# Optimization experiments

Measured on AMD Instinct MI355X. Metric: run time of the kernel, lower is better.

Reference implementation:

```python
import jax, jax.numpy as jnp
import numpy as np

B, N, NPOINT, NSAMPLE, C = 8, 8192, 2048, 32, 64
RADIUS = 0.2
MLP = [C + 3, 64, 64, 128]  # use_xyz=True -> C+3 input channels


def setup_inputs() -> dict:
    key = jax.random.key(0)
    ks = jax.random.split(key, 8)
    xyz = jax.random.normal(ks[0], (B, N, 3), jnp.float32)
    features = jax.random.normal(ks[1], (B, C, N), jnp.float32)
    inp = {"xyz": xyz, "features": features}
    # shared-MLP (1x1 conv) weights, He-init
    for i in range(3):
        cin, cout = MLP[i], MLP[i + 1]
        scale = jnp.sqrt(jnp.float32(2.0) / cin)
        inp[f"W{i+1}"] = jax.random.normal(ks[2 + i], (cout, cin), jnp.float32) * scale
        inp[f"b{i+1}"] = jnp.zeros((cout,), jnp.float32)
    return inp


def furthest_point_sample(xyz, npoint):
    # xyz: (B, N, 3) -> idx: (B, npoint). Greedy FPS, seeded at point 0 (as CUDA impl).
    b, n, _ = xyz.shape

    def step(carry, _):
        dist, far = carry  # dist: (B, N) running min dist-to-set; far: (B,)
        centroid = jnp.take_along_axis(xyz, far[:, None, None], axis=1)  # (B,1,3)
        d = jnp.sum((xyz - centroid) ** 2, axis=-1)  # (B, N)
        dist = jnp.minimum(dist, d)
        nxt = jnp.argmax(dist, axis=-1).astype(jnp.int32)
        return (dist, nxt), far

    init = (jnp.full((b, n), jnp.inf, xyz.dtype), jnp.zeros((b,), jnp.int32))
    _, idx = jax.lax.scan(step, init, None, length=npoint)  # (npoint, B)
    return idx.T  # (B, npoint)


def ball_query(xyz, new_xyz, radius, nsample):
    # xyz: (B,N,3), new_xyz: (B,S,3) -> idx: (B,S,nsample)
    n = xyz.shape[1]
    d2 = jnp.sum((new_xyz[:, :, None, :] - xyz[:, None, :, :]) ** 2, axis=-1)  # (B,S,N)
    inball = d2 < jnp.float32(radius) ** 2
    keys = jnp.where(inball, jnp.arange(n, dtype=jnp.int32), jnp.int32(n))
    neg_small, _ = jax.lax.top_k(-keys, nsample)  # nsample smallest indices in ball
    idx = -neg_small  # (B,S,nsample), padded with n where fewer than nsample
    first = idx[..., :1]
    idx = jnp.where(idx == n, first, idx)  # repeat first valid neighbor (CUDA semantics)
    idx = jnp.where(idx == n, 0, idx)  # empty ball -> index 0
    return idx


def reference(xyz, features, W1, b1, W2, b2, W3, b3):
    # --- sample: FPS + gather centers (non-differentiable index selection) ---
    fps_idx = furthest_point_sample(jax.lax.stop_gradient(xyz), NPOINT)  # (B,S)
    new_xyz = jnp.take_along_axis(xyz, fps_idx[:, :, None], axis=1)  # (B,S,3)

    # --- group: ball query + gather neighbors, relative coords, concat feats ---
    idx = ball_query(jax.lax.stop_gradient(xyz), jax.lax.stop_gradient(new_xyz),
                     RADIUS, NSAMPLE)  # (B,S,K)
    batch_ix = jnp.arange(B)[:, None, None]
    grouped_xyz = xyz[batch_ix, idx] - new_xyz[:, :, None, :]  # (B,S,K,3)
    feats_n = jnp.swapaxes(features, 1, 2)  # (B,N,C)
    grouped_feats = feats_n[batch_ix, idx]  # (B,S,K,C)
    x = jnp.concatenate([grouped_xyz, grouped_feats], axis=-1)  # (B,S,K,C+3)

    # --- shared MLP (1x1 convs + ReLU) ---
    x = jax.nn.relu(jnp.einsum('bskc,oc->bsko', x, W1) + b1)
    x = jax.nn.relu(jnp.einsum('bskc,oc->bsko', x, W2) + b2)
    x = jax.nn.relu(jnp.einsum('bskc,oc->bsko', x, W3) + b3)

    # --- max-pool over neighborhood K ---
    new_features = jnp.max(x, axis=2)  # (B,S,out)
    new_features = jnp.swapaxes(new_features, 1, 2)  # (B,out,S)
    return new_xyz, new_features
```

## Files before the change

### kernel.cpp

```cpp
#include <hip/hip_runtime.h>

#define BB 8
#define NN 8192
#define NPOINT 2048
#define NSAMPLE 32
#define CC 64

typedef float v2f __attribute__((ext_vector_type(2)));

__global__ __launch_bounds__(256) void k_transpose(const float* __restrict__ f,
                                                   float* __restrict__ ft) {
  __shared__ float tile[64][65];
  int b = blockIdx.y;
  int p0 = blockIdx.x * 64;
  int tx = threadIdx.x, ty = threadIdx.y;
  const float* fb = f + (size_t)b * CC * NN;
#pragma unroll
  for (int i = 0; i < 16; ++i) {
    int c = i * 4 + ty;
    tile[c][tx] = fb[(size_t)c * NN + p0 + tx];
  }
  __syncthreads();
  float* fo = ft + ((size_t)b * NN + p0) * CC;
#pragma unroll
  for (int i = 0; i < 16; ++i) {
    int pl = i * 4 + ty;
    fo[(size_t)pl * CC + tx] = tile[tx][pl];
  }
}

__global__ void k_permW1(const float* __restrict__ W1, float* __restrict__ W1p) {
  int i = blockIdx.x * 256 + threadIdx.x;
  if (i < 64 * 68) {
    int o = i / 68, k = i % 68;
    float v;
    if (k < 64) v = W1[o * 67 + 3 + k];
    else if (k < 67) v = W1[o * 67 + (k - 64)];
    else v = 0.0f;
    W1p[i] = v;
  }
}

#define DPP_STAGE(ctrl)                                                         \
  {                                                                             \
    unsigned long long _b = (unsigned long long)__double_as_longlong(best);     \
    int _lo = __builtin_amdgcn_update_dpp(0, (int)(unsigned)_b, ctrl, 0xf, 0xf, \
                                          false);                               \
    int _hi = __builtin_amdgcn_update_dpp(0, (int)(unsigned)(_b >> 32), ctrl,   \
                                          0xf, 0xf, false);                     \
    double _s = __longlong_as_double(                                           \
        (long long)(((unsigned long long)(unsigned)_hi << 32) | (unsigned)_lo));\
    best = fmax(best, _s);                                                      \
  }

__global__ __launch_bounds__(512, 2) void k_fps(const float* __restrict__ xyz,
                                                float* __restrict__ newxyz) {
  __shared__ float sx[NN], sy[NN], sz[NN];
  __shared__ float swin[3 * NPOINT];
  __shared__ __align__(16) double wkey[2][8];
  int b = blockIdx.x;
  const float* X = xyz + (size_t)b * NN * 3;
  int t = threadIdx.x;
  v2f px[8], py[8], pz[8], dd[8];
#pragma unroll
  for (int j = 0; j < 8; ++j) {
    int p0 = t + (2 * j) * 512, p1 = p0 + 512;
    float x0 = X[p0 * 3 + 0], y0 = X[p0 * 3 + 1], z0 = X[p0 * 3 + 2];
    float x1 = X[p1 * 3 + 0], y1 = X[p1 * 3 + 1], z1 = X[p1 * 3 + 2];
    px[j].x = x0; px[j].y = x1;
    py[j].x = y0; py[j].y = y1;
    pz[j].x = z0; pz[j].y = z1;
    sx[p0] = x0; sy[p0] = y0; sz[p0] = z0;
    sx[p1] = x1; sy[p1] = y1; sz[p1] = z1;
    dd[j].x = __builtin_inff(); dd[j].y = __builtin_inff();
  }
  __syncthreads();
  float cx = sx[0], cy = sy[0], cz = sz[0];
  if (t == 0) { swin[0] = cx; swin[1] = cy; swin[2] = cz; }
  for (int it = 1; it < NPOINT; ++it) {
#pragma clang fp contract(off)
    v2f vcx, vcy, vcz;
    vcx.x = cx; vcx.y = cx;
    vcy.x = cy; vcy.y = cy;
    vcz.x = cz; vcz.y = cz;
    float m0 = -1.0f, m1 = -1.0f;
    int k0 = 0, k1 = 0;
#pragma unroll
    for (int j = 0; j < 8; ++j) {
      v2f dx = px[j] - vcx;
      v2f dy = py[j] - vcy;
      v2f dz = pz[j] - vcz;
      v2f xx = dx * dx;
      v2f yy = dy * dy;
      v2f zz = dz * dz;
      v2f s = xx + yy;
      v2f d = s + zz;
      v2f nd = __builtin_elementwise_min(dd[j], d);
      dd[j] = nd;
      if (nd.x > m0) { m0 = nd.x; k0 = j; }
      if (nd.y > m1) { m1 = nd.y; k1 = j; }
    }
    unsigned i0 = (unsigned)(t + (k0 << 10));
    unsigned i1 = (unsigned)(t + (k1 << 10) + 512);
    double best = __longlong_as_double(
        (long long)(((unsigned long long)__float_as_uint(m0) << 32) | ~i0));
    double c1 = __longlong_as_double(
        (long long)(((unsigned long long)__float_as_uint(m1) << 32) | ~i1));
    best = fmax(best, c1);
    DPP_STAGE(0x111)
    DPP_STAGE(0x112)
    DPP_STAGE(0x114)
    DPP_STAGE(0x118)
    DPP_STAGE(0x142)
    DPP_STAGE(0x143)
    int sel = it & 1;
    if ((t & 63) == 63) wkey[sel][t >> 6] = best;
    __syncthreads();
    double2 a0 = *(const double2*)&wkey[sel][0];
    double2 a1 = *(const double2*)&wkey[sel][2];
    double2 a2 = *(const double2*)&wkey[sel][4];
    double2 a3 = *(const double2*)&wkey[sel][6];
    double g = fmax(fmax(fmax(a0.x, a0.y), fmax(a1.x, a1.y)),
                    fmax(fmax(a2.x, a2.y), fmax(a3.x, a3.y)));
    unsigned wi = ~(unsigned)(unsigned long long)__double_as_longlong(g);
    cx = sx[wi]; cy = sy[wi]; cz = sz[wi];
    if (t == 0) {
      swin[3 * it + 0] = cx;
      swin[3 * it + 1] = cy;
      swin[3 * it + 2] = cz;
    }
  }
  __syncthreads();
  float* ob = newxyz + (size_t)b * 3 * NPOINT;
#pragma unroll
  for (int i = 0; i < 12; ++i) ob[t + i * 512] = swin[t + i * 512];
}

__global__ __launch_bounds__(256) void k_ballq(const float* __restrict__ xyz,
                                               const float* __restrict__ newxyz,
                                               int* __restrict__ idxout) {
  __shared__ int lidx[4][32];
  int w = threadIdx.x >> 6, lane = threadIdx.x & 63;
  int g = blockIdx.x * 4 + w;
  int b = g >> 11, s = g & 2047;
  const float* X = xyz + (size_t)b * NN * 3;
  const float* c = newxyz + ((size_t)b * NPOINT + s) * 3;
  float cx = c[0], cy = c[1], cz = c[2];
  const float r2 = 0.2f * 0.2f;
  int found = 0;
  for (int ch = 0; ch < NN / 64; ++ch) {
    int p = ch * 64 + lane;
    float x = X[p * 3 + 0], y = X[p * 3 + 1], z = X[p * 3 + 2];
    float dx = __fsub_rn(cx, x);
    float dy = __fsub_rn(cy, y);
    float dz = __fsub_rn(cz, z);
    float d2 = __fadd_rn(__fadd_rn(__fmul_rn(dx, dx), __fmul_rn(dy, dy)),
                         __fmul_rn(dz, dz));
    bool in = d2 < r2;
    unsigned long long m = __ballot(in);
    int rank = __popcll(m & ((1ull << lane) - 1ull));
    int slot = found + rank;
    if (in && slot < NSAMPLE) lidx[w][slot] = p;
    found += __popcll(m);
    if (found >= NSAMPLE) break;
  }
  int nf = found < NSAMPLE ? found : NSAMPLE;
  if (lane < NSAMPLE) {
    int v = (nf == 0) ? 0 : lidx[w][lane < nf ? lane : 0];
    idxout[(size_t)g * NSAMPLE + lane] = v;
  }
}

__global__ __launch_bounds__(256) void k_mlp(
    const float* __restrict__ featsT, const float* __restrict__ xyz,
    const float* __restrict__ newxyz, const int* __restrict__ idx,
    const float* __restrict__ W1p, const float* __restrict__ b1,
    const float* __restrict__ W2, const float* __restrict__ b2,
    const float* __restrict__ W3, const float* __restrict__ b3,
    float* __restrict__ outf) {
  __shared__ __align__(16) float xb[4][32][68];
  int w = threadIdx.x >> 6, lane = threadIdx.x & 63;
  int g = blockIdx.x * 4 + w;
  int b = g >> 11, s2 = g & 2047;

  {
    int sl = lane & 31, half = lane >> 5;
    int p = idx[(size_t)g * NSAMPLE + sl];
    const float4* src = (const float4*)(featsT + (((size_t)b << 13) + p) * 64);
    float4* dst = (float4*)&xb[w][sl][0];
    if (half == 0) {
#pragma unroll
      for (int kt = 0; kt < 8; ++kt) dst[kt] = src[kt];
    } else {
#pragma unroll
      for (int kt = 8; kt < 16; ++kt) dst[kt] = src[kt];
      const float* cp = newxyz + (((size_t)b << 11) + s2) * 3;
      const float* pp = xyz + (((size_t)b << 13) + p) * 3;
      float dx = __fsub_rn(pp[0], cp[0]);
      float dy = __fsub_rn(pp[1], cp[1]);
      float dz = __fsub_rn(pp[2], cp[2]);
      dst[16] = make_float4(dx, dy, dz, 0.0f);
    }
  }
  int si = lane & 3, oi = lane >> 2;
  float* xrow0 = &xb[w][0][0];
  float acc[4][8];

#pragma unroll
  for (int r = 0; r < 4; ++r) {
    float bv = b1[oi * 4 + r];
#pragma unroll
    for (int q = 0; q < 8; ++q) acc[r][q] = bv;
  }
  for (int kt = 0; kt < 17; ++kt) {
    float4 wv[4];
#pragma unroll
    for (int r = 0; r < 4; ++r)
      wv[r] = *(const float4*)(W1p + (oi * 4 + r) * 68 + kt * 4);
#pragma unroll
    for (int q = 0; q < 8; ++q) {
      float4 xv = *(const float4*)(xrow0 + (si + 4 * q) * 68 + kt * 4);
#pragma unroll
      for (int r = 0; r < 4; ++r) {
        acc[r][q] = fmaf(wv[r].x, xv.x, acc[r][q]);
        acc[r][q] = fmaf(wv[r].y, xv.y, acc[r][q]);
        acc[r][q] = fmaf(wv[r].z, xv.z, acc[r][q]);
        acc[r][q] = fmaf(wv[r].w, xv.w, acc[r][q]);
      }
    }
  }
#pragma unroll
  for (int q = 0; q < 8; ++q) {
    int s = si + 4 * q;
    float4 v = make_float4(fmaxf(acc[0][q], 0.f), fmaxf(acc[1][q], 0.f),
                           fmaxf(acc[2][q], 0.f), fmaxf(acc[3][q], 0.f));
    *(float4*)(xrow0 + s * 68 + oi * 4) = v;
  }

#pragma unroll
  for (int r = 0; r < 4; ++r) {
    float bv = b2[oi * 4 + r];
#pragma unroll
    for (int q = 0; q < 8; ++q) acc[r][q] = bv;
  }
  for (int kt = 0; kt < 16; ++kt) {
    float4 wv[4];
#pragma unroll
    for (int r = 0; r < 4; ++r)
      wv[r] = *(const float4*)(W2 + (oi * 4 + r) * 64 + kt * 4);
#pragma unroll
    for (int q = 0; q < 8; ++q) {
      float4 xv = *(const float4*)(xrow0 + (si + 4 * q) * 68 + kt * 4);
#pragma unroll
      for (int r = 0; r < 4; ++r) {
        acc[r][q] = fmaf(wv[r].x, xv.x, acc[r][q]);
        acc[r][q] = fmaf(wv[r].y, xv.y, acc[r][q]);
        acc[r][q] = fmaf(wv[r].z, xv.z, acc[r][q]);
        acc[r][q] = fmaf(wv[r].w, xv.w, acc[r][q]);
      }
    }
  }
#pragma unroll
  for (int q = 0; q < 8; ++q) {
    int s = si + 4 * q;
    float4 v = make_float4(fmaxf(acc[0][q], 0.f), fmaxf(acc[1][q], 0.f),
                           fmaxf(acc[2][q], 0.f), fmaxf(acc[3][q], 0.f));
    *(float4*)(xrow0 + s * 68 + oi * 4) = v;
  }

  float accB[4][8];
#pragma unroll
  for (int r = 0; r < 4; ++r) {
    float bvA = b3[oi * 4 + r];
    float bvB = b3[64 + oi * 4 + r];
#pragma unroll
    for (int q = 0; q < 8; ++q) { acc[r][q] = bvA; accB[r][q] = bvB; }
  }
  for (int kt = 0; kt < 16; ++kt) {
    float4 wa[4], wb[4];
#pragma unroll
    for (int r = 0; r < 4; ++r) {
      wa[r] = *(const float4*)(W3 + (oi * 4 + r) * 64 + kt * 4);
      wb[r] = *(const float4*)(W3 + (64 + oi * 4 + r) * 64 + kt * 4);
    }
#pragma unroll
    for (int q = 0; q < 8; ++q) {
      float4 xv = *(const float4*)(xrow0 + (si + 4 * q) * 68 + kt * 4);
#pragma unroll
      for (int r = 0; r < 4; ++r) {
        acc[r][q] = fmaf(wa[r].x, xv.x, acc[r][q]);
        acc[r][q] = fmaf(wa[r].y, xv.y, acc[r][q]);
        acc[r][q] = fmaf(wa[r].z, xv.z, acc[r][q]);
        acc[r][q] = fmaf(wa[r].w, xv.w, acc[r][q]);
        accB[r][q] = fmaf(wb[r].x, xv.x, accB[r][q]);
        accB[r][q] = fmaf(wb[r].y, xv.y, accB[r][q]);
        accB[r][q] = fmaf(wb[r].z, xv.z, accB[r][q]);
        accB[r][q] = fmaf(wb[r].w, xv.w, accB[r][q]);
      }
    }
  }
#pragma unroll
  for (int r = 0; r < 4; ++r) {
    float mA = acc[r][0], mB = accB[r][0];
#pragma unroll
    for (int q = 1; q < 8; ++q) {
      mA = fmaxf(mA, acc[r][q]);
      mB = fmaxf(mB, accB[r][q]);
    }
    mA = fmaxf(mA, __shfl_xor(mA, 1));
    mA = fmaxf(mA, __shfl_xor(mA, 2));
    mB = fmaxf(mB, __shfl_xor(mB, 1));
    mB = fmaxf(mB, __shfl_xor(mB, 2));
    mA = fmaxf(mA, 0.0f);
    mB = fmaxf(mB, 0.0f);
    if (si == 0) {
      int o = oi * 4 + r;
      outf[(((size_t)b * 128 + o) << 11) + s2] = mA;
      outf[(((size_t)b * 128 + o + 64) << 11) + s2] = mB;
    }
  }
}

extern "C" void kernel_launch(void* const* d_in, const int* in_sizes, int n_in,
                              void* d_out, int out_size, void* d_ws, size_t ws_size,
                              hipStream_t stream) {
  const float* xyz = (const float*)d_in[0];
  const float* feats = (const float*)d_in[1];
  const float* W1 = (const float*)d_in[2];
  const float* b1 = (const float*)d_in[3];
  const float* W2 = (const float*)d_in[4];
  const float* b2 = (const float*)d_in[5];
  const float* W3 = (const float*)d_in[6];
  const float* b3 = (const float*)d_in[7];
  float* out_newxyz = (float*)d_out;
  float* out_feats = (float*)d_out + (size_t)BB * NPOINT * 3;

  char* ws = (char*)d_ws;
  float* featsT = (float*)ws;
  float* W1p = (float*)(ws + 16777216);
  int* idx = (int*)(ws + 16777216 + 17408);

  dim3 tb(64, 4);
  k_transpose<<<dim3(NN / 64, BB), tb, 0, stream>>>(feats, featsT);
  k_permW1<<<17, 256, 0, stream>>>(W1, W1p);
  k_fps<<<BB, 512, 0, stream>>>(xyz, out_newxyz);
  k_ballq<<<(BB * NPOINT) / 4, 256, 0, stream>>>(xyz, out_newxyz, idx);
  k_mlp<<<(BB * NPOINT) / 4, 256, 0, stream>>>(featsT, xyz, out_newxyz, idx,
                                               W1p, b1, W2, b2, W3, b3, out_feats);
}
```

Before: 2.042 ms.

## Shrink FPS block to 4 waves with DPP cross-wave reduce; fuse ball query into MLP

The FPS kernel drops from 512 to 256 threads, so each thread holds 32 points and there are four waves instead of eight. The cross-wave argmax is now read from a 4-entry LDS array and reduced with quad-permute DPP rather than scalar fmax chains. Point coordinates are packed as float4 in LDS, so the winner lookup is a single load. The ball query is fused into the MLP kernel, which removes a launch and the index round-trip through global memory, at the cost of doubling per-thread FPS work and serial ALU.

```diff
diff --git a/kernel.cpp b/kernel.cpp
--- a/kernel.cpp
+++ b/kernel.cpp
@@ -52,30 +52,46 @@
         (long long)(((unsigned long long)(unsigned)_hi << 32) | (unsigned)_lo));\
     best = fmax(best, _s);                                                      \
   }
-
-__global__ __launch_bounds__(512, 2) void k_fps(const float* __restrict__ xyz,
+#define QP_STAGE(ctrl)                                                          \
+  {                                                                             \
+    unsigned long long _b = (unsigned long long)__double_as_longlong(gk);       \
+    int _lo = __builtin_amdgcn_update_dpp(0, (int)(unsigned)_b, ctrl, 0xf, 0xf, \
+                                          false);                               \
+    int _hi = __builtin_amdgcn_update_dpp(0, (int)(unsigned)(_b >> 32), ctrl,   \
+                                          0xf, 0xf, false);                     \
+    double _s = __longlong_as_double(                                           \
+        (long long)(((unsigned long long)(unsigned)_hi << 32) | (unsigned)_lo));\
+    gk = fmax(gk, _s);                                                          \
+  }
+
+__global__ __launch_bounds__(256, 1) void k_fps(const float* __restrict__ xyz,
                                                 float* __restrict__ newxyz) {
-  __shared__ float sx[NN], sy[NN], sz[NN];
+  __shared__ __align__(16) float4 sxyz[NN];
   __shared__ float swin[3 * NPOINT];
-  __shared__ __align__(16) double wkey[2][8];
+  __shared__ __align__(16) double wkey[2][4];
   int b = blockIdx.x;
   const float* X = xyz + (size_t)b * NN * 3;
   int t = threadIdx.x;
-  v2f px[8], py[8], pz[8], dd[8];
-#pragma unroll
-  for (int j = 0; j < 8; ++j) {
-    int p0 = t + (2 * j) * 512, p1 = p0 + 512;
+  int lane = t & 63;
+  v2f px[16], py[16], pz[16], dd[16];
+#pragma unroll
+  for (int j = 0; j < 16; ++j) {
+    int p0 = t + (2 * j) * 256, p1 = p0 + 256;
     float x0 = X[p0 * 3 + 0], y0 = X[p0 * 3 + 1], z0 = X[p0 * 3 + 2];
     float x1 = X[p1 * 3 + 0], y1 = X[p1 * 3 + 1], z1 = X[p1 * 3 + 2];
     px[j].x = x0; px[j].y = x1;
     py[j].x = y0; py[j].y = y1;
     pz[j].x = z0; pz[j].y = z1;
-    sx[p0] = x0; sy[p0] = y0; sz[p0] = z0;
-    sx[p1] = x1; sy[p1] = y1; sz[p1] = z1;
+    sxyz[p0] = make_float4(x0, y0, z0, 0.0f);
+    sxyz[p1] = make_float4(x1, y1, z1, 0.0f);
     dd[j].x = __builtin_inff(); dd[j].y = __builtin_inff();
   }
   __syncthreads();
-  float cx = sx[0], cy = sy[0], cz = sz[0];
+  float cx, cy, cz;
+  {
+    float4 c0 = sxyz[0];
+    cx = c0.x; cy = c0.y; cz = c0.z;
+  }
   if (t == 0) { swin[0] = cx; swin[1] = cy; swin[2] = cz; }
   for (int it = 1; it < NPOINT; ++it) {
 #pragma clang fp contract(off)
@@ -86,7 +102,7 @@
     float m0 = -1.0f, m1 = -1.0f;
     int k0 = 0, k1 = 0;
 #pragma unroll
-    for (int j = 0; j < 8; ++j) {
+    for (int j = 0; j < 16; ++j) {
       v2f dx = px[j] - vcx;
       v2f dy = py[j] - vcy;
       v2f dz = pz[j] - vcz;
@@ -100,8 +116,8 @@
       if (nd.x > m0) { m0 = nd.x; k0 = j; }
       if (nd.y > m1) { m1 = nd.y; k1 = j; }
     }
-    unsigned i0 = (unsigned)(t + (k0 << 10));
-    unsigned i1 = (unsigned)(t + (k1 << 10) + 512);
+    unsigned i0 = (unsigned)(t + (k0 << 9));
+    unsigned i1 = (unsigned)(t + (k1 << 9) + 256);
     double best = __longlong_as_double(
         (long long)(((unsigned long long)__float_as_uint(m0) << 32) | ~i0));
     double c1 = __longlong_as_double(
@@ -114,16 +130,14 @@
     DPP_STAGE(0x142)
     DPP_STAGE(0x143)
     int sel = it & 1;
-    if ((t & 63) == 63) wkey[sel][t >> 6] = best;
+    if (lane == 63) wkey[sel][t >> 6] = best;
     __syncthreads();
-    double2 a0 = *(const double2*)&wkey[sel][0];
-    double2 a1 = *(const double2*)&wkey[sel][2];
-    double2 a2 = *(const double2*)&wkey[sel][4];
-    double2 a3 = *(const double2*)&wkey[sel][6];
-    double g = fmax(fmax(fmax(a0.x, a0.y), fmax(a1.x, a1.y)),
-                    fmax(fmax(a2.x, a2.y), fmax(a3.x, a3.y)));
-    unsigned wi = ~(unsigned)(unsigned long long)__double_as_longlong(g);
-    cx = sx[wi]; cy = sy[wi]; cz = sz[wi];
+    double gk = wkey[sel][lane & 3];
+    QP_STAGE(0xB1)
+    QP_STAGE(0x4E)
+    unsigned wi = ~(unsigned)(unsigned long long)__double_as_longlong(gk);
+    float4 cw = sxyz[wi];
+    cx = cw.x; cy = cw.y; cz = cw.z;
     if (t == 0) {
       swin[3 * it + 0] = cx;
       swin[3 * it + 1] = cy;
@@ -133,59 +147,47 @@
   __syncthreads();
   float* ob = newxyz + (size_t)b * 3 * NPOINT;
 #pragma unroll
-  for (int i = 0; i < 12; ++i) ob[t + i * 512] = swin[t + i * 512];
-}
-
-__global__ __launch_bounds__(256) void k_ballq(const float* __restrict__ xyz,
-                                               const float* __restrict__ newxyz,
-                                               int* __restrict__ idxout) {
-  __shared__ int lidx[4][32];
-  int w = threadIdx.x >> 6, lane = threadIdx.x & 63;
-  int g = blockIdx.x * 4 + w;
-  int b = g >> 11, s = g & 2047;
-  const float* X = xyz + (size_t)b * NN * 3;
-  const float* c = newxyz + ((size_t)b * NPOINT + s) * 3;
-  float cx = c[0], cy = c[1], cz = c[2];
-  const float r2 = 0.2f * 0.2f;
-  int found = 0;
-  for (int ch = 0; ch < NN / 64; ++ch) {
-    int p = ch * 64 + lane;
-    float x = X[p * 3 + 0], y = X[p * 3 + 1], z = X[p * 3 + 2];
-    float dx = __fsub_rn(cx, x);
-    float dy = __fsub_rn(cy, y);
-    float dz = __fsub_rn(cz, z);
-    float d2 = __fadd_rn(__fadd_rn(__fmul_rn(dx, dx), __fmul_rn(dy, dy)),
-                         __fmul_rn(dz, dz));
-    bool in = d2 < r2;
-    unsigned long long m = __ballot(in);
-    int rank = __popcll(m & ((1ull << lane) - 1ull));
-    int slot = found + rank;
-    if (in && slot < NSAMPLE) lidx[w][slot] = p;
-    found += __popcll(m);
-    if (found >= NSAMPLE) break;
-  }
-  int nf = found < NSAMPLE ? found : NSAMPLE;
-  if (lane < NSAMPLE) {
-    int v = (nf == 0) ? 0 : lidx[w][lane < nf ? lane : 0];
-    idxout[(size_t)g * NSAMPLE + lane] = v;
-  }
+  for (int i = 0; i < 24; ++i) ob[t + i * 256] = swin[t + i * 256];
 }
 
 __global__ __launch_bounds__(256) void k_mlp(
     const float* __restrict__ featsT, const float* __restrict__ xyz,
-    const float* __restrict__ newxyz, const int* __restrict__ idx,
+    const float* __restrict__ newxyz,
     const float* __restrict__ W1p, const float* __restrict__ b1,
     const float* __restrict__ W2, const float* __restrict__ b2,
     const float* __restrict__ W3, const float* __restrict__ b3,
     float* __restrict__ outf) {
   __shared__ __align__(16) float xb[4][32][68];
+  __shared__ int lidx[4][32];
   int w = threadIdx.x >> 6, lane = threadIdx.x & 63;
   int g = blockIdx.x * 4 + w;
   int b = g >> 11, s2 = g & 2047;
+  const float* X = xyz + (size_t)b * NN * 3;
+  const float* cp = newxyz + (((size_t)b << 11) + s2) * 3;
+  float ccx = cp[0], ccy = cp[1], ccz = cp[2];
 
   {
+    const float r2 = 0.2f * 0.2f;
+    int found = 0;
+    for (int ch = 0; ch < NN / 64; ++ch) {
+      int p = ch * 64 + lane;
+      float x = X[p * 3 + 0], y = X[p * 3 + 1], z = X[p * 3 + 2];
+      float dx = __fsub_rn(ccx, x);
+      float dy = __fsub_rn(ccy, y);
+      float dz = __fsub_rn(ccz, z);
+      float d2 = __fadd_rn(__fadd_rn(__fmul_rn(dx, dx), __fmul_rn(dy, dy)),
+                           __fmul_rn(dz, dz));
+      bool in = d2 < r2;
+      unsigned long long m = __ballot(in);
+      int rank = __popcll(m & ((1ull << lane) - 1ull));
+      int slot = found + rank;
+      if (in && slot < NSAMPLE) lidx[w][slot] = p;
+      found += __popcll(m);
+      if (found >= NSAMPLE) break;
+    }
+    int nf = found < NSAMPLE ? found : NSAMPLE;
     int sl = lane & 31, half = lane >> 5;
-    int p = idx[(size_t)g * NSAMPLE + sl];
+    int p = (nf == 0) ? 0 : lidx[w][sl < nf ? sl : 0];
     const float4* src = (const float4*)(featsT + (((size_t)b << 13) + p) * 64);
     float4* dst = (float4*)&xb[w][sl][0];
     if (half == 0) {
@@ -194,11 +196,10 @@
     } else {
 #pragma unroll
       for (int kt = 8; kt < 16; ++kt) dst[kt] = src[kt];
-      const float* cp = newxyz + (((size_t)b << 11) + s2) * 3;
-      const float* pp = xyz + (((size_t)b << 13) + p) * 3;
-      float dx = __fsub_rn(pp[0], cp[0]);
-      float dy = __fsub_rn(pp[1], cp[1]);
-      float dz = __fsub_rn(pp[2], cp[2]);
+      const float* pp = X + p * 3;
+      float dx = __fsub_rn(pp[0], ccx);
+      float dy = __fsub_rn(pp[1], ccy);
+      float dz = __fsub_rn(pp[2], ccz);
       dst[16] = make_float4(dx, dy, dz, 0.0f);
     }
   }
@@ -338,13 +339,11 @@
   char* ws = (char*)d_ws;
   float* featsT = (float*)ws;
   float* W1p = (float*)(ws + 16777216);
-  int* idx = (int*)(ws + 16777216 + 17408);
 
   dim3 tb(64, 4);
   k_transpose<<<dim3(NN / 64, BB), tb, 0, stream>>>(feats, featsT);
   k_permW1<<<17, 256, 0, stream>>>(W1, W1p);
-  k_fps<<<BB, 512, 0, stream>>>(xyz, out_newxyz);
-  k_ballq<<<(BB * NPOINT) / 4, 256, 0, stream>>>(xyz, out_newxyz, idx);
-  k_mlp<<<(BB * NPOINT) / 4, 256, 0, stream>>>(featsT, xyz, out_newxyz, idx,
+  k_fps<<<BB, 256, 0, stream>>>(xyz, out_newxyz);
+  k_mlp<<<(BB * NPOINT) / 4, 256, 0, stream>>>(featsT, xyz, out_newxyz,
                                                W1p, b1, W2, b2, W3, b3, out_feats);
 }
```

Result: faster. 1.997 ms (-2.2%).
